# Kernel tuning notes

Measured on AMD Instinct MI355X. Metric: run time of the kernel, lower is better.

## Reference

```python
import jax, jax.numpy as jnp
import numpy as np

N = 100000   # nodes per graph
E = 1200000  # edges per graph
D_IN = 64
FILTERS = [128, 128, 64]
K_SLICES = 16
MLP = [32, 16, 8, 4]


def setup_inputs() -> dict:
    key = jax.random.key(0)
    ks = jax.random.split(key, 24)
    s = 0.1
    inp = {
        'x_i': jax.random.normal(ks[0], (N, D_IN), jnp.float32),
        'edge_index_i': jax.random.randint(ks[1], (2, E), 0, N, jnp.int64),
        'x_j': jax.random.normal(ks[2], (N, D_IN), jnp.float32),
        'edge_index_j': jax.random.randint(ks[3], (2, E), 0, N, jnp.int64),
    }
    # GCN conv stack params: 64->128->128->64
    dims = [D_IN] + FILTERS
    for li in range(3):
        inp[f'conv_w{li}'] = jax.random.normal(ks[4 + 2 * li], (dims[li], dims[li + 1]), jnp.float32) * s
        inp[f'conv_b{li}'] = jnp.zeros((dims[li + 1],), jnp.float32)
    d = FILTERS[-1]
    inp['att_w'] = jax.random.normal(ks[10], (d, d), jnp.float32) * s
    inp['ntn_wt'] = jax.random.normal(ks[11], (K_SLICES, d, d), jnp.float32) * s
    inp['ntn_wm'] = jax.random.normal(ks[12], (K_SLICES, 2 * d), jnp.float32) * s
    inp['ntn_b'] = jnp.zeros((K_SLICES,), jnp.float32)
    mdims = [K_SLICES] + MLP
    for li in range(4):
        inp[f'mlp_w{li}'] = jax.random.normal(ks[13 + 2 * li], (mdims[li], mdims[li + 1]), jnp.float32) * s
        inp[f'mlp_b{li}'] = jnp.zeros((mdims[li + 1],), jnp.float32)
    inp['score_w'] = jax.random.normal(ks[22], (MLP[-1], 1), jnp.float32) * s
    inp['score_b'] = jnp.zeros((1,), jnp.float32)
    return inp


def _gcn(x, W, b, src, dst):
    # PyG GCNConv: add self loops, symmetric normalization, aggregate into dst.
    n = x.shape[0]
    loop = jnp.arange(n, dtype=src.dtype)
    src = jnp.concatenate([src, loop])
    dst = jnp.concatenate([dst, loop])
    deg = jax.ops.segment_sum(jnp.ones_like(dst, dtype=x.dtype), dst, num_segments=n)
    dinv = jax.lax.rsqrt(deg)  # deg >= 1 due to self loops
    norm = dinv[src] * dinv[dst]             # [E+N]
    xw = x @ W                               # [N, Dout]
    out = jax.ops.segment_sum(xw[src] * norm[:, None], dst, num_segments=n)
    return out + b


def _attention(x, Wa):
    # global context attention pooling over nodes
    gc = jnp.tanh(jnp.mean(x @ Wa, axis=0))          # [D]
    att = jax.nn.sigmoid(x @ gc)                     # [N]
    return jnp.sum(x * att[:, None], axis=0)         # [D]


def _ntn(h_i, h_j, Wt, Wm, b):
    # s_k = h_i^T Wt[k] h_j + Wm[k] . [h_i; h_j] + b_k, then tanh
    bilinear = jnp.einsum('d,kde,e->k', h_i, Wt, h_j)
    linear = Wm @ jnp.concatenate([h_i, h_j])
    return jnp.tanh(bilinear + linear + b)           # [K]


def reference(x_i, edge_index_i, x_j, edge_index_j,
              conv_w0, conv_b0, conv_w1, conv_b1, conv_w2, conv_b2,
              att_w, ntn_wt, ntn_wm, ntn_b,
              mlp_w0, mlp_b0, mlp_w1, mlp_b1, mlp_w2, mlp_b2, mlp_w3, mlp_b3,
              score_w, score_b):
    convs = [(conv_w0, conv_b0), (conv_w1, conv_b1), (conv_w2, conv_b2)]
    si, di = edge_index_i[0], edge_index_i[1]
    sj, dj = edge_index_j[0], edge_index_j[1]
    for li, (W, b) in enumerate(convs):
        x_i = _gcn(x_i, W, b, si, di)
        x_j = _gcn(x_j, W, b, sj, dj)
        if li < len(convs) - 1:
            x_i = jax.nn.relu(x_i)
            x_j = jax.nn.relu(x_j)
    h_i = _attention(x_i, att_w)
    h_j = _attention(x_j, att_w)
    z = _ntn(h_i, h_j, ntn_wt, ntn_wm, ntn_b)        # [K]
    for W, b in [(mlp_w0, mlp_b0), (mlp_w1, mlp_b1), (mlp_w2, mlp_b2), (mlp_w3, mlp_b3)]:
        z = jax.nn.relu(z @ W + b)
    return z @ score_w + score_b                     # [1]
```

## Files before the change

kernel.cpp:

```cpp
#include <hip/hip_runtime.h>
#include <cstdint>
#include <cstddef>

#define CDIV(a,b) (((a)+(b)-1)/(b))

typedef __attribute__((ext_vector_type(8))) unsigned short ushort8v;
typedef __attribute__((ext_vector_type(8))) short short8v;
typedef __attribute__((ext_vector_type(4))) float f32x4;

constexpr int BCAP = 8192;
constexpr int CPAD = 256 * BCAP;

__device__ __forceinline__ float bf2f(unsigned short u) {
  return __uint_as_float(((unsigned)u) << 16);
}
__device__ __forceinline__ unsigned short f2bf(float f) {
  unsigned u = __float_as_uint(f);
  unsigned r = (u + 0x7fff + ((u >> 16) & 1)) >> 16;
  return (unsigned short)r;
}


__global__ void k_prep(const float* __restrict__ w0, const float* __restrict__ w1,
                       const float* __restrict__ w2,
                       unsigned short* __restrict__ w0p, unsigned short* __restrict__ w1p,
                       unsigned short* __restrict__ w2p,
                       int* __restrict__ gcur, double* __restrict__ gcsum,
                       double* __restrict__ hsum) {
  int id = blockIdx.x * 256 + threadIdx.x;
  if (id < 512) gcur[id] = 0;
  else if (id < 640) gcsum[id - 512] = 0.0;
  else if (id < 768) hsum[id - 640] = 0.0;
  if (id < 8192) {
    int k = id / 128, n = id % 128;
    w0p[n * 64 + ((((k >> 3) + n) & 7) * 8) + (k & 7)] = f2bf(w0[id]);
  }
  if (id < 16384) {
    int k = id / 128, n = id % 128;
    w1p[n * 128 + ((((k >> 3) + n) & 15) * 8) + (k & 7)] = f2bf(w1[id]);
  }
  if (id < 8192) {
    int k = id / 64, n = id % 64;
    w2p[n * 128 + ((((k >> 3) + n) & 15) * 8) + (k & 7)] = f2bf(w2[id]);
  }
}


__global__ __launch_bounds__(256) void k_place(const int* __restrict__ src0,
                                               const int* __restrict__ dst0,
                                               const int* __restrict__ src1,
                                               const int* __restrict__ dst1,
                                               int E, int N,
                                               int* __restrict__ gcur,
                                               unsigned* __restrict__ part) {
  __shared__ int bcnt[256], bbase[256], bcur[256];
  int g = blockIdx.y;
  const int* src = g ? src1 : src0;
  const int* dst = g ? dst1 : dst0;
  int t = threadIdx.x;
  int e0 = blockIdx.x * 4096, e1 = min(e0 + 4096, E);
  bcnt[t] = 0;
  __syncthreads();
  for (int e = e0 + t; e < e1; e += 256) atomicAdd(&bcnt[dst[e] >> 9], 1);
  __syncthreads();
  bbase[t] = t * BCAP + (bcnt[t] ? atomicAdd(&gcur[g * 256 + t], bcnt[t]) : 0);
  bcur[t] = 0;
  __syncthreads();
  unsigned* pg = part + (size_t)g * CPAD;
  for (int e = e0 + t; e < e1; e += 256) {
    int d = dst[e], s = src[e];
    int b = d >> 9;
    int off = atomicAdd(&bcur[b], 1);
    pg[bbase[b] + off] = ((unsigned)(d & 511) << 18) | (unsigned)(s + g * N);
  }
}


__global__ __launch_bounds__(256) void k_build(const unsigned* __restrict__ part,
                                               const int* __restrict__ gcur,
                                               int2* __restrict__ rowp2, int* __restrict__ col,
                                               float* __restrict__ dinv, int n) {
  __shared__ int cnt[512], off[512], tmp[256];
  int g = blockIdx.y, b = blockIdx.x;
  int lo = b << 9;
  if (lo >= n) return;
  int t = threadIdx.x;
  int s0 = b * BCAP;
  int cntE = gcur[g * 256 + b];
  const unsigned* pg = part + (size_t)g * CPAD;
  cnt[t] = 0; cnt[t + 256] = 0;
  __syncthreads();
  for (int e = s0 + t; e < s0 + cntE; e += 256) atomicAdd(&cnt[pg[e] >> 18], 1);
  __syncthreads();
  int a0 = cnt[2 * t], a1 = cnt[2 * t + 1];
  int ps = a0 + a1;
  tmp[t] = ps; __syncthreads();
  for (int o = 1; o < 256; o <<= 1) {
    int x = (t >= o) ? tmp[t - o] : 0;
    __syncthreads();
    tmp[t] += x;
    __syncthreads();
  }
  int ex = tmp[t] - ps;
  off[2 * t] = ex;
  off[2 * t + 1] = ex + a0;
  __syncthreads();
  for (int i = t; i < 512; i += 256) {
    int node = lo + i;
    if (node < n) {
      int st = g * CPAD + s0 + off[i];
      rowp2[g * n + node] = make_int2(st, st + cnt[i]);
      dinv[g * n + node] = rsqrtf((float)(cnt[i] + 1));
    }
  }
  __syncthreads();
  for (int e = s0 + t; e < s0 + cntE; e += 256) {
    unsigned pr = pg[e];
    int p = atomicAdd(&off[pr >> 18], 1);
    col[g * CPAD + s0 + p] = (int)(pr & 0x3FFFFu);
  }
}


__global__ void k_tobf(const float* __restrict__ in0, const float* __restrict__ in1,
                       const float* __restrict__ dinv,
                       unsigned short* __restrict__ out, int n8half, int n8) {
  int i = blockIdx.x * blockDim.x + threadIdx.x;
  if (i < n8) {
    const float4* i4 = (i < n8half) ? (const float4*)in0 : (const float4*)in1;
    int ii = (i < n8half) ? i : i - n8half;
    float di = dinv[i >> 3];
    float4 a = i4[2 * ii], b = i4[2 * ii + 1];
    ushort8v r;
    r[0] = f2bf(di * a.x); r[1] = f2bf(di * a.y); r[2] = f2bf(di * a.z); r[3] = f2bf(di * a.w);
    r[4] = f2bf(di * b.x); r[5] = f2bf(di * b.y); r[6] = f2bf(di * b.z); r[7] = f2bf(di * b.w);
    ((ushort8v*)out)[i] = r;
  }
}


template<int D, bool ADD_BIAS, bool COLSUM>
__device__ __forceinline__ void agg_body(
    const unsigned short* __restrict__ xin, unsigned short* __restrict__ xout,
    const int2* __restrict__ rowp2, const int* __restrict__ col,
    const float* __restrict__ dinv, const float* __restrict__ bias, int n,
    float* __restrict__ partial) {
  constexpr int G = D / 8;
  constexpr int NPB = 256 / G;
  int node = blockIdx.x * NPB + threadIdx.x / G;
  int g = threadIdx.x % G;
  const ushort8v* x8 = (const ushort8v*)xin;
  float r[8];
  if (node < n) {
    float di = dinv[node];
    float acc[8];
    {
      ushort8v xs = x8[(size_t)node * G + g];
#pragma unroll
      for (int j = 0; j < 8; ++j) acc[j] = bf2f(xs[j]);
    }
    int2 rp = rowp2[node];
    int e = rp.x, e1 = rp.y;
    for (; e + 4 <= e1; e += 4) {
      int s0 = col[e], s1 = col[e + 1], s2 = col[e + 2], s3 = col[e + 3];
      ushort8v v0 = x8[(size_t)s0 * G + g];
      ushort8v v1 = x8[(size_t)s1 * G + g];
      ushort8v v2 = x8[(size_t)s2 * G + g];
      ushort8v v3 = x8[(size_t)s3 * G + g];
#pragma unroll
      for (int j = 0; j < 8; ++j) {
        acc[j] += bf2f(v0[j]); acc[j] += bf2f(v1[j]);
        acc[j] += bf2f(v2[j]); acc[j] += bf2f(v3[j]);
      }
    }
    for (; e < e1; ++e) {
      int s = col[e];
      ushort8v v = x8[(size_t)s * G + g];
#pragma unroll
      for (int j = 0; j < 8; ++j) acc[j] += bf2f(v[j]);
    }
#pragma unroll
    for (int j = 0; j < 8; ++j) {
      r[j] = di * acc[j];
      if (ADD_BIAS) r[j] += bias[g * 8 + j];
    }
    ushort8v o;
#pragma unroll
    for (int j = 0; j < 8; ++j) o[j] = f2bf(r[j]);
    ((ushort8v*)xout)[(size_t)node * G + g] = o;
  } else {
#pragma unroll
    for (int j = 0; j < 8; ++j) r[j] = 0.f;
  }
  if (COLSUM) {
    __shared__ float ws[4][64];
    int lane = threadIdx.x & 63, wave = threadIdx.x >> 6;
#pragma unroll
    for (int j = 0; j < 8; ++j) {
      float v = r[j];
      v += __shfl_xor(v, 8);
      v += __shfl_xor(v, 16);
      v += __shfl_xor(v, 32);
      r[j] = v;
    }
    if (lane < 8) {
#pragma unroll
      for (int j = 0; j < 8; ++j) ws[wave][lane * 8 + j] = r[j];
    }
    __syncthreads();
    int t = threadIdx.x;
    if (t < 64) partial[(size_t)blockIdx.x * 64 + t] = ws[0][t] + ws[1][t] + ws[2][t] + ws[3][t];
  }
}

__global__ __launch_bounds__(256) void k_aggL0(
    const unsigned short* __restrict__ x, unsigned short* __restrict__ o,
    const int2* __restrict__ rp, const int* __restrict__ col,
    const float* __restrict__ dv, int n) {
  agg_body<64, false, false>(x, o, rp, col, dv, nullptr, n, nullptr);
}
__global__ __launch_bounds__(256) void k_aggL1(
    const unsigned short* __restrict__ x, unsigned short* __restrict__ o,
    const int2* __restrict__ rp, const int* __restrict__ col,
    const float* __restrict__ dv, int n) {
  agg_body<128, false, false>(x, o, rp, col, dv, nullptr, n, nullptr);
}
__global__ __launch_bounds__(256) void k_aggF(
    const unsigned short* __restrict__ x, unsigned short* __restrict__ o,
    const int2* __restrict__ rp, const int* __restrict__ col,
    const float* __restrict__ dv, const float* __restrict__ bias, int n,
    float* __restrict__ partial) {
  agg_body<64, true, true>(x, o, rp, col, dv, bias, n, partial);
}


template<int K, int DOUT, bool RELU, bool PRESCALE>
__device__ __forceinline__ void gemm_body(
    const unsigned short* __restrict__ A, const unsigned short* __restrict__ Wp,
    const float* __restrict__ bias, unsigned short* __restrict__ C,
    const float* __restrict__ dinv, int n) {
  constexpr int CPR = K / 8;
  constexpr int CM = CPR - 1;
  constexpr int NT = DOUT / 16;
  __shared__ unsigned short As[128 * K];
  __shared__ unsigned short Ws[DOUT * K];
  int t = threadIdx.x;
  int blockM = blockIdx.x * 128;

#pragma unroll
  for (int id = t; id < 128 * CPR; id += 256) {
    int r = id / CPR, c = id % CPR;
    int grow = blockM + r;
    ushort8v v = {0, 0, 0, 0, 0, 0, 0, 0};
    if (grow < n) v = ((const ushort8v*)A)[(size_t)grow * CPR + c];
    *(ushort8v*)&As[r * K + ((c + r) & CM) * 8] = v;
  }
#pragma unroll
  for (int id = t; id < DOUT * CPR; id += 256)
    ((ushort8v*)Ws)[id] = ((const ushort8v*)Wp)[id];
  __syncthreads();

  int lane = t & 63, wave = t >> 6;
  int m15 = lane & 15, quad = lane >> 4;
  f32x4 acc[2][NT];
#pragma unroll
  for (int i = 0; i < 2; ++i)
#pragma unroll
    for (int j = 0; j < NT; ++j) acc[i][j] = (f32x4){0.f, 0.f, 0.f, 0.f};

  int i0 = wave * 32 + m15;
  int i1 = i0 + 16;
#pragma unroll
  for (int kc = 0; kc < K; kc += 32) {
    int c0 = (kc >> 3) + quad;
    short8v a0 = *(const short8v*)&As[i0 * K + ((c0 + i0) & CM) * 8];
    short8v a1 = *(const short8v*)&As[i1 * K + ((c0 + i1) & CM) * 8];
    short8v b[NT];
#pragma unroll
    for (int nt = 0; nt < NT; ++nt) {
      int nn = nt * 16 + m15;
      b[nt] = *(const short8v*)&Ws[nn * K + ((c0 + nn) & CM) * 8];
    }
#pragma unroll
    for (int nt = 0; nt < NT; ++nt) {
      acc[0][nt] = __builtin_amdgcn_mfma_f32_16x16x32_bf16(a0, b[nt], acc[0][nt], 0, 0, 0);
      acc[1][nt] = __builtin_amdgcn_mfma_f32_16x16x32_bf16(a1, b[nt], acc[1][nt], 0, 0, 0);
    }
  }

#pragma unroll
  for (int rt = 0; rt < 2; ++rt) {
    int rbase = blockM + wave * 32 + rt * 16 + quad * 4;
#pragma unroll
    for (int nt = 0; nt < NT; ++nt) {
      int colg = nt * 16 + m15;
      float bv = bias ? bias[colg] : 0.f;
#pragma unroll
      for (int r = 0; r < 4; ++r) {
        int row = rbase + r;
        if (row < n) {
          float v = acc[rt][nt][r] + bv;
          if (RELU) v = fmaxf(v, 0.f);
          if (PRESCALE) v *= dinv[row];
          C[(size_t)row * DOUT + colg] = f2bf(v);
        }
      }
    }
  }
}

__global__ __launch_bounds__(256) void k_gemmL0(
    const unsigned short* __restrict__ A, const unsigned short* __restrict__ Wp,
    const float* __restrict__ bias, unsigned short* __restrict__ C,
    const float* __restrict__ dv, int n) {
  gemm_body<64, 128, true, true>(A, Wp, bias, C, dv, n);
}
__global__ __launch_bounds__(256) void k_gemmL1(
    const unsigned short* __restrict__ A, const unsigned short* __restrict__ Wp,
    const float* __restrict__ bias, unsigned short* __restrict__ C,
    const float* __restrict__ dv, int n) {
  gemm_body<128, 128, true, false>(A, Wp, bias, C, dv, n);
}
__global__ __launch_bounds__(256) void k_gemmL2(
    const unsigned short* __restrict__ A, const unsigned short* __restrict__ Wp,
    const float* __restrict__ bias, unsigned short* __restrict__ C,
    const float* __restrict__ dv, int n) {
  gemm_body<128, 64, false, true>(A, Wp, bias, C, dv, n);
}


__global__ __launch_bounds__(256) void k_cm2(const float* __restrict__ partial, int nbg,
                                             double* __restrict__ gcsum) {
  __shared__ double sd[256];
  int g = blockIdx.y, t = threadIdx.x;
  int f = t & 63, rg = t >> 6;
  double acc = 0.0;
  for (int b = blockIdx.x * 4 + rg; b < nbg; b += gridDim.x * 4)
    acc += (double)partial[(size_t)(g * nbg + b) * 64 + f];
  sd[t] = acc; __syncthreads();
  if (t < 64) {
    double tot = sd[t] + sd[t + 64] + sd[t + 128] + sd[t + 192];
    atomicAdd(&gcsum[g * 64 + t], tot);
  }
}


__global__ void k_hsum(const unsigned short* __restrict__ x, const double* __restrict__ gcsum,
                       const float* __restrict__ Wa, int N, int n2,
                       double* __restrict__ hsum) {
  __shared__ float m[128], gcs[128];
  __shared__ double sd[256][4];
  int t = threadIdx.x;
  if (t < 128) m[t] = (float)(gcsum[t] / (double)N);
  __syncthreads();
  if (t < 128) {
    int gg = t >> 6, f = t & 63;
    float s = 0.f;
    for (int d = 0; d < 64; ++d) s += m[gg * 64 + d] * Wa[d * 64 + f];
    gcs[t] = tanhf(s);
  }
  __syncthreads();
  int g = t & 15, sub = t >> 4;
  float4 gcv0 = ((const float4*)gcs)[g];
  float4 gcv1 = ((const float4*)gcs)[16 + g];
  double a[2][4];
#pragma unroll
  for (int j = 0; j < 4; ++j) { a[0][j] = 0.0; a[1][j] = 0.0; }
  for (int node = blockIdx.x * 16 + sub; node < n2; node += gridDim.x * 16) {
    int gid = node >= N;
    float4 gcv = gid ? gcv1 : gcv0;
    ushort4 xu = ((const ushort4*)x)[(size_t)node * 16 + g];
    float x0 = bf2f(xu.x), x1 = bf2f(xu.y), x2 = bf2f(xu.z), x3 = bf2f(xu.w);
    float p = x0 * gcv.x + x1 * gcv.y + x2 * gcv.z + x3 * gcv.w;
    p += __shfl_xor(p, 1);
    p += __shfl_xor(p, 2);
    p += __shfl_xor(p, 4);
    p += __shfl_xor(p, 8);
    float att = 1.f / (1.f + expf(-p));
    a[gid][0] += (double)(att * x0); a[gid][1] += (double)(att * x1);
    a[gid][2] += (double)(att * x2); a[gid][3] += (double)(att * x3);
  }
#pragma unroll 1
  for (int gid = 0; gid < 2; ++gid) {
    sd[t][0] = a[gid][0]; sd[t][1] = a[gid][1];
    sd[t][2] = a[gid][2]; sd[t][3] = a[gid][3];
    __syncthreads();
    if (t < 64) {
      int gg = t >> 2, j = t & 3;
      double tot = 0;
      for (int w = 0; w < 16; ++w) tot += sd[w * 16 + gg][j];
      if (tot != 0.0) atomicAdd(&hsum[gid * 64 + t], tot);
    }
    __syncthreads();
  }
}


__global__ __launch_bounds__(1024) void k_final(
    const double* __restrict__ hsum,
    const float* __restrict__ Wt, const float* __restrict__ Wm,
    const float* __restrict__ bn,
    const float* __restrict__ w0, const float* __restrict__ b0,
    const float* __restrict__ w1, const float* __restrict__ b1,
    const float* __restrict__ w2, const float* __restrict__ b2,
    const float* __restrict__ w3, const float* __restrict__ b3,
    const float* __restrict__ sw, const float* __restrict__ sb,
    float* __restrict__ out) {
  __shared__ float hi[64], hj[64], red[1024], z[16], u[32], v[16], w[8], q[4];
  int t = threadIdx.x;
  if (t < 64) hi[t] = (float)hsum[t];
  else if (t < 128) hj[t - 64] = (float)hsum[t];
  __syncthreads();
  int k = t >> 6, r = t & 63;
  const float* wr = Wt + ((size_t)k * 64 + r) * 64;
  float s = 0.f;
#pragma unroll 8
  for (int c = 0; c < 64; ++c) s += wr[c] * hj[c];
  float p = hi[r] * s;
  p += Wm[k * 128 + r] * hi[r] + Wm[k * 128 + 64 + r] * hj[r];
  red[t] = p;
  __syncthreads();
  for (int o = 32; o > 0; o >>= 1) {
    if (r < o) red[t] += red[t + o];
    __syncthreads();
  }
  if (t < 16) z[t] = tanhf(red[t * 64] + bn[t]);
  __syncthreads();
  if (t < 32) {
    float ss = b0[t];
    for (int i = 0; i < 16; ++i) ss += z[i] * w0[i * 32 + t];
    u[t] = fmaxf(ss, 0.f);
  }
  __syncthreads();
  if (t < 16) {
    float ss = b1[t];
    for (int i = 0; i < 32; ++i) ss += u[i] * w1[i * 16 + t];
    v[t] = fmaxf(ss, 0.f);
  }
  __syncthreads();
  if (t < 8) {
    float ss = b2[t];
    for (int i = 0; i < 16; ++i) ss += v[i] * w2[i * 8 + t];
    w[t] = fmaxf(ss, 0.f);
  }
  __syncthreads();
  if (t < 4) {
    float ss = b3[t];
    for (int i = 0; i < 8; ++i) ss += w[i] * w3[i * 4 + t];
    q[t] = fmaxf(ss, 0.f);
  }
  __syncthreads();
  if (t == 0) {
    float ss = sb[0];
    for (int i = 0; i < 4; ++i) ss += q[i] * sw[i];
    out[0] = ss;
  }
}


extern "C" void kernel_launch(void* const* d_in, const int* in_sizes, int n_in,
                              void* d_out, int out_size, void* d_ws, size_t ws_size,
                              hipStream_t stream) {
  const float* x_i = (const float*)d_in[0];
  const int*   ei  = (const int*)d_in[1];
  const float* x_j = (const float*)d_in[2];
  const int*   ej  = (const int*)d_in[3];
  const float* cw0 = (const float*)d_in[4];  const float* cb0 = (const float*)d_in[5];
  const float* cw1 = (const float*)d_in[6];  const float* cb1 = (const float*)d_in[7];
  const float* cw2 = (const float*)d_in[8];  const float* cb2 = (const float*)d_in[9];
  const float* aw  = (const float*)d_in[10];
  const float* wt  = (const float*)d_in[11]; const float* wm  = (const float*)d_in[12];
  const float* bn  = (const float*)d_in[13];
  const float* m0w = (const float*)d_in[14]; const float* m0b = (const float*)d_in[15];
  const float* m1w = (const float*)d_in[16]; const float* m1b = (const float*)d_in[17];
  const float* m2w = (const float*)d_in[18]; const float* m2b = (const float*)d_in[19];
  const float* m3w = (const float*)d_in[20]; const float* m3b = (const float*)d_in[21];
  const float* sw  = (const float*)d_in[22]; const float* sb  = (const float*)d_in[23];

  int N = in_sizes[0] / 64;
  int E = in_sizes[1] / 2;
  int N2 = 2 * N;

  char* p = (char*)d_ws;
  auto alloc = [&](size_t b) -> void* {
    void* r = (void*)p;
    p += (b + 255) & ~(size_t)255;
    return r;
  };
  int*    gcur    = (int*)alloc(512 * 4);
  double* gcsum   = (double*)alloc(128 * 8);
  double* hsum    = (double*)alloc(128 * 8);
  int2*   rowp2   = (int2*)alloc((size_t)N2 * 8);
  int*    col     = (int*)alloc((size_t)2 * CPAD * 4);
  float*  dinv    = (float*)alloc((size_t)N2 * 4);
  float*  partial = (float*)alloc((size_t)CDIV(N2, 32) * 64 * 4);
  unsigned short* w0p = (unsigned short*)alloc(64 * 128 * 2);
  unsigned short* w1p = (unsigned short*)alloc(128 * 128 * 2);
  unsigned short* w2p = (unsigned short*)alloc(128 * 64 * 2);
  char* S1 = (char*)alloc((size_t)N2 * 128 * 2);
  char* S2 = (char*)alloc((size_t)N2 * 128 * 2);

  k_prep<<<64, 256, 0, stream>>>(cw0, cw1, cw2, w0p, w1p, w2p, gcur, gcsum, hsum);

  unsigned* part = (unsigned*)S1;
  k_place<<<dim3(CDIV(E, 4096), 2), 256, 0, stream>>>(ei, ei + E, ej, ej + E, E, N, gcur, part);
  k_build<<<dim3(256, 2), 256, 0, stream>>>(part, gcur, rowp2, col, dinv, N);

  unsigned short* xbf = (unsigned short*)S2;
  k_tobf<<<CDIV(N2 * 8, 256), 256, 0, stream>>>(x_i, x_j, dinv, xbf, N * 8, N2 * 8);

  unsigned short* A0 = (unsigned short*)S1;
  unsigned short* G0 = (unsigned short*)S2;
  unsigned short* A1 = (unsigned short*)S1;
  unsigned short* G1 = (unsigned short*)S2;
  unsigned short* G2 = (unsigned short*)S1;
  unsigned short* F = (unsigned short*)S2;

  k_aggL0<<<CDIV(N2, 32), 256, 0, stream>>>(xbf, A0, rowp2, col, dinv, N2);
  k_gemmL0<<<CDIV(N2, 128), 256, 0, stream>>>(A0, w0p, cb0, G0, dinv, N2);
  k_aggL1<<<CDIV(N2, 16), 256, 0, stream>>>(G0, A1, rowp2, col, dinv, N2);
  k_gemmL1<<<CDIV(N2, 128), 256, 0, stream>>>(A1, w1p, cb1, G1, dinv, N2);
  k_gemmL2<<<CDIV(N2, 128), 256, 0, stream>>>(G1, w2p, nullptr, G2, dinv, N2);
  k_aggF<<<CDIV(N2, 32), 256, 0, stream>>>(G2, F, rowp2, col, dinv, cb2, N2, partial);

  k_cm2<<<dim3(32, 2), 256, 0, stream>>>(partial, N / 32, gcsum);
  k_hsum<<<1024, 256, 0, stream>>>(F, gcsum, aw, N, N2, hsum);

  k_final<<<1, 1024, 0, stream>>>(hsum, wt, wm, bn,
                                  m0w, m0b, m1w, m1b, m2w, m2b, m3w, m3b,
                                  sw, sb, (float*)d_out);
}
```

Baseline: 565.1 us.

## Store gathered node features in FP8 to halve gather bandwidth

Inputs to the three aggregation kernels are now stored as FP8 (e4m3 via the packed convert builtins) instead of bf16. This covers the initial feature conversion and the outputs of gemmL0 and gemmL2, and the gather loop decodes them with the packed fp8-to-f32 convert. The aim is to halve the bytes moved by the random neighbour gathers, which dominate the aggregation cost. The trade-off is much lower precision, which risks breaking accuracy tolerance. The gemm epilogue also now writes single bytes, which are narrow and poorly coalesced stores.

```diff
diff --git a/kernel.cpp b/kernel.cpp
--- a/kernel.cpp
+++ b/kernel.cpp
@@ -7,6 +7,7 @@
 typedef __attribute__((ext_vector_type(8))) unsigned short ushort8v;
 typedef __attribute__((ext_vector_type(8))) short short8v;
 typedef __attribute__((ext_vector_type(4))) float f32x4;
+typedef __attribute__((ext_vector_type(2))) float f32x2;
 
 constexpr int BCAP = 8192;
 constexpr int CPAD = 256 * BCAP;
@@ -18,6 +19,14 @@
   unsigned u = __float_as_uint(f);
   unsigned r = (u + 0x7fff + ((u >> 16) & 1)) >> 16;
   return (unsigned short)r;
+}
+
+__device__ __forceinline__ void acc_fp8(float* acc, uint2 v) {
+  f32x2 p;
+  p = __builtin_amdgcn_cvt_pk_f32_fp8((int)v.x, false); acc[0] += p[0]; acc[1] += p[1];
+  p = __builtin_amdgcn_cvt_pk_f32_fp8((int)v.x, true);  acc[2] += p[0]; acc[3] += p[1];
+  p = __builtin_amdgcn_cvt_pk_f32_fp8((int)v.y, false); acc[4] += p[0]; acc[5] += p[1];
+  p = __builtin_amdgcn_cvt_pk_f32_fp8((int)v.y, true);  acc[6] += p[0]; acc[7] += p[1];
 }
 
 
@@ -122,26 +131,27 @@
 }
 
 
-__global__ void k_tobf(const float* __restrict__ in0, const float* __restrict__ in1,
-                       const float* __restrict__ dinv,
-                       unsigned short* __restrict__ out, int n8half, int n8) {
+__global__ void k_tofp8(const float* __restrict__ in0, const float* __restrict__ in1,
+                        const float* __restrict__ dinv,
+                        uint2* __restrict__ out, int n8half, int n8) {
   int i = blockIdx.x * blockDim.x + threadIdx.x;
   if (i < n8) {
     const float4* i4 = (i < n8half) ? (const float4*)in0 : (const float4*)in1;
     int ii = (i < n8half) ? i : i - n8half;
     float di = dinv[i >> 3];
     float4 a = i4[2 * ii], b = i4[2 * ii + 1];
-    ushort8v r;
-    r[0] = f2bf(di * a.x); r[1] = f2bf(di * a.y); r[2] = f2bf(di * a.z); r[3] = f2bf(di * a.w);
-    r[4] = f2bf(di * b.x); r[5] = f2bf(di * b.y); r[6] = f2bf(di * b.z); r[7] = f2bf(di * b.w);
-    ((ushort8v*)out)[i] = r;
+    int lo = __builtin_amdgcn_cvt_pk_fp8_f32(di * a.x, di * a.y, 0, false);
+    lo = __builtin_amdgcn_cvt_pk_fp8_f32(di * a.z, di * a.w, lo, true);
+    int hi = __builtin_amdgcn_cvt_pk_fp8_f32(di * b.x, di * b.y, 0, false);
+    hi = __builtin_amdgcn_cvt_pk_fp8_f32(di * b.z, di * b.w, hi, true);
+    out[i] = make_uint2((unsigned)lo, (unsigned)hi);
   }
 }
 
 
 template<int D, bool ADD_BIAS, bool COLSUM>
 __device__ __forceinline__ void agg_body(
-    const unsigned short* __restrict__ xin, unsigned short* __restrict__ xout,
+    const unsigned char* __restrict__ xin, unsigned short* __restrict__ xout,
     const int2* __restrict__ rowp2, const int* __restrict__ col,
     const float* __restrict__ dinv, const float* __restrict__ bias, int n,
     float* __restrict__ partial) {
@@ -149,35 +159,28 @@
   constexpr int NPB = 256 / G;
   int node = blockIdx.x * NPB + threadIdx.x / G;
   int g = threadIdx.x % G;
-  const ushort8v* x8 = (const ushort8v*)xin;
+  const uint2* x8 = (const uint2*)xin;
   float r[8];
   if (node < n) {
     float di = dinv[node];
     float acc[8];
-    {
-      ushort8v xs = x8[(size_t)node * G + g];
-#pragma unroll
-      for (int j = 0; j < 8; ++j) acc[j] = bf2f(xs[j]);
-    }
+#pragma unroll
+    for (int j = 0; j < 8; ++j) acc[j] = 0.f;
+    acc_fp8(acc, x8[(size_t)node * G + g]);
     int2 rp = rowp2[node];
     int e = rp.x, e1 = rp.y;
     for (; e + 4 <= e1; e += 4) {
       int s0 = col[e], s1 = col[e + 1], s2 = col[e + 2], s3 = col[e + 3];
-      ushort8v v0 = x8[(size_t)s0 * G + g];
-      ushort8v v1 = x8[(size_t)s1 * G + g];
-      ushort8v v2 = x8[(size_t)s2 * G + g];
-      ushort8v v3 = x8[(size_t)s3 * G + g];
-#pragma unroll
-      for (int j = 0; j < 8; ++j) {
-        acc[j] += bf2f(v0[j]); acc[j] += bf2f(v1[j]);
-        acc[j] += bf2f(v2[j]); acc[j] += bf2f(v3[j]);
-      }
+      uint2 v0 = x8[(size_t)s0 * G + g];
+      uint2 v1 = x8[(size_t)s1 * G + g];
+      uint2 v2 = x8[(size_t)s2 * G + g];
+      uint2 v3 = x8[(size_t)s3 * G + g];
+      acc_fp8(acc, v0); acc_fp8(acc, v1);
+      acc_fp8(acc, v2); acc_fp8(acc, v3);
     }
     for (; e < e1; ++e) {
       int s = col[e];
-      ushort8v v = x8[(size_t)s * G + g];
-#pragma unroll
-      for (int j = 0; j < 8; ++j) acc[j] += bf2f(v[j]);
+      acc_fp8(acc, x8[(size_t)s * G + g]);
     }
 #pragma unroll
     for (int j = 0; j < 8; ++j) {
@@ -214,19 +217,19 @@
 }
 
 __global__ __launch_bounds__(256) void k_aggL0(
-    const unsigned short* __restrict__ x, unsigned short* __restrict__ o,
+    const unsigned char* __restrict__ x, unsigned short* __restrict__ o,
     const int2* __restrict__ rp, const int* __restrict__ col,
     const float* __restrict__ dv, int n) {
   agg_body<64, false, false>(x, o, rp, col, dv, nullptr, n, nullptr);
 }
 __global__ __launch_bounds__(256) void k_aggL1(
-    const unsigned short* __restrict__ x, unsigned short* __restrict__ o,
+    const unsigned char* __restrict__ x, unsigned short* __restrict__ o,
     const int2* __restrict__ rp, const int* __restrict__ col,
     const float* __restrict__ dv, int n) {
   agg_body<128, false, false>(x, o, rp, col, dv, nullptr, n, nullptr);
 }
 __global__ __launch_bounds__(256) void k_aggF(
-    const unsigned short* __restrict__ x, unsigned short* __restrict__ o,
+    const unsigned char* __restrict__ x, unsigned short* __restrict__ o,
     const int2* __restrict__ rp, const int* __restrict__ col,
     const float* __restrict__ dv, const float* __restrict__ bias, int n,
     float* __restrict__ partial) {
@@ -234,10 +237,10 @@
 }
 
 
-template<int K, int DOUT, bool RELU, bool PRESCALE>
+template<int K, int DOUT, bool RELU, bool PRESCALE, bool OUTFP8>
 __device__ __forceinline__ void gemm_body(
     const unsigned short* __restrict__ A, const unsigned short* __restrict__ Wp,
-    const float* __restrict__ bias, unsigned short* __restrict__ C,
+    const float* __restrict__ bias, void* __restrict__ Cv,
     const float* __restrict__ dinv, int n) {
   constexpr int CPR = K / 8;
   constexpr int CM = CPR - 1;
@@ -302,7 +305,12 @@
           float v = acc[rt][nt][r] + bv;
           if (RELU) v = fmaxf(v, 0.f);
           if (PRESCALE) v *= dinv[row];
-          C[(size_t)row * DOUT + colg] = f2bf(v);
+          if (OUTFP8) {
+            int b8 = __builtin_amdgcn_cvt_pk_fp8_f32(v, v, 0, false);
+            ((unsigned char*)Cv)[(size_t)row * DOUT + colg] = (unsigned char)(b8 & 0xff);
+          } else {
+            ((unsigned short*)Cv)[(size_t)row * DOUT + colg] = f2bf(v);
+          }
         }
       }
     }
@@ -311,21 +319,21 @@
 
 __global__ __launch_bounds__(256) void k_gemmL0(
     const unsigned short* __restrict__ A, const unsigned short* __restrict__ Wp,
-    const float* __restrict__ bias, unsigned short* __restrict__ C,
+    const float* __restrict__ bias, void* __restrict__ C,
     const float* __restrict__ dv, int n) {
-  gemm_body<64, 128, true, true>(A, Wp, bias, C, dv, n);
+  gemm_body<64, 128, true, true, true>(A, Wp, bias, C, dv, n);
 }
 __global__ __launch_bounds__(256) void k_gemmL1(
     const unsigned short* __restrict__ A, const unsigned short* __restrict__ Wp,
-    const float* __restrict__ bias, unsigned short* __restrict__ C,
+    const float* __restrict__ bias, void* __restrict__ C,
     const float* __restrict__ dv, int n) {
-  gemm_body<128, 128, true, false>(A, Wp, bias, C, dv, n);
+  gemm_body<128, 128, true, false, false>(A, Wp, bias, C, dv, n);
 }
 __global__ __launch_bounds__(256) void k_gemmL2(
     const unsigned short* __restrict__ A, const unsigned short* __restrict__ Wp,
-    const float* __restrict__ bias, unsigned short* __restrict__ C,
+    const float* __restrict__ bias, void* __restrict__ C,
     const float* __restrict__ dv, int n) {
-  gemm_body<128, 64, false, true>(A, Wp, bias, C, dv, n);
+  gemm_body<128, 64, false, true, true>(A, Wp, bias, C, dv, n);
 }
 
 
@@ -506,17 +514,17 @@
   k_place<<<dim3(CDIV(E, 4096), 2), 256, 0, stream>>>(ei, ei + E, ej, ej + E, E, N, gcur, part);
   k_build<<<dim3(256, 2), 256, 0, stream>>>(part, gcur, rowp2, col, dinv, N);
 
-  unsigned short* xbf = (unsigned short*)S2;
-  k_tobf<<<CDIV(N2 * 8, 256), 256, 0, stream>>>(x_i, x_j, dinv, xbf, N * 8, N2 * 8);
+  unsigned char* xf8 = (unsigned char*)S2;
+  k_tofp8<<<CDIV(N2 * 8, 256), 256, 0, stream>>>(x_i, x_j, dinv, (uint2*)xf8, N * 8, N2 * 8);
 
   unsigned short* A0 = (unsigned short*)S1;
-  unsigned short* G0 = (unsigned short*)S2;
+  unsigned char*  G0 = (unsigned char*)S2;
   unsigned short* A1 = (unsigned short*)S1;
   unsigned short* G1 = (unsigned short*)S2;
-  unsigned short* G2 = (unsigned short*)S1;
-  unsigned short* F = (unsigned short*)S2;
-
-  k_aggL0<<<CDIV(N2, 32), 256, 0, stream>>>(xbf, A0, rowp2, col, dinv, N2);
+  unsigned char*  G2 = (unsigned char*)S1;
+  unsigned short* F  = (unsigned short*)S2;
+
+  k_aggL0<<<CDIV(N2, 32), 256, 0, stream>>>(xf8, A0, rowp2, col, dinv, N2);
   k_gemmL0<<<CDIV(N2, 128), 256, 0, stream>>>(A0, w0p, cb0, G0, dinv, N2);
   k_aggL1<<<CDIV(N2, 16), 256, 0, stream>>>(G0, A1, rowp2, col, dinv, N2);
   k_gemmL1<<<CDIV(N2, 128), 256, 0, stream>>>(A1, w1p, cb1, G1, dinv, N2);
```

Result: faster. 509.1 us (-9.9%).
